# Kernel optimization log

Measured on AMD Instinct MI355X. Metric: run time of the kernel, lower is better.

The kernel has to match this reference:

```python
import jax, jax.numpy as jnp
import numpy as np

DIM = 2048
N_HEADS = 16
HEAD_DIM = DIM // N_HEADS
ROPE_BASE = 10000.0


def _rope_cos_sin(seq_len, head_dim, dtype):
    inv_freq = 1.0 / (ROPE_BASE ** (jnp.arange(0, head_dim, 2, dtype=jnp.float32) / head_dim))
    t = jnp.arange(seq_len, dtype=jnp.float32)
    freqs = jnp.einsum('s,d->sd', t, inv_freq)          # (S, hd/2)
    emb = jnp.concatenate([freqs, freqs], axis=-1)       # (S, hd)
    return jnp.cos(emb).astype(dtype), jnp.sin(emb).astype(dtype)


def _rotate_half(x):
    x1, x2 = jnp.split(x, 2, axis=-1)
    return jnp.concatenate([-x2, x1], axis=-1)


def _apply_rope(x, cos, sin):
    # x: (B, H, S, hd); cos/sin: (S, hd)
    return x * cos[None, None] + _rotate_half(x) * sin[None, None]


def setup_inputs() -> dict:
    key = jax.random.key(0)
    ks = jax.random.split(key, 5)
    B, S = 2, 2048
    scale = 1.0 / np.sqrt(DIM)
    return {
        'x': jax.random.normal(ks[0], (B, S, DIM), dtype=jnp.float32),
        'Wq': jax.random.normal(ks[1], (DIM, DIM), dtype=jnp.float32) * scale,
        'Wk': jax.random.normal(ks[2], (DIM, DIM), dtype=jnp.float32) * scale,
        'Wv': jax.random.normal(ks[3], (DIM, DIM), dtype=jnp.float32) * scale,
        'Wo': jax.random.normal(ks[4], (DIM, DIM), dtype=jnp.float32) * scale,
    }


def reference(x, Wq, Wk, Wv, Wo):
    B, S, _ = x.shape
    scale = HEAD_DIM ** -0.5

    def proj(W):
        # torch Linear: x @ W.T ; reshape to (B, H, S, hd)
        return (x @ W.T).reshape(B, S, N_HEADS, HEAD_DIM).transpose(0, 2, 1, 3)

    q, k, v = proj(Wq), proj(Wk), proj(Wv)
    cos, sin = _rope_cos_sin(S, HEAD_DIM, x.dtype)
    q = _apply_rope(q, cos, sin)
    k = _apply_rope(k, cos, sin)

    scores = jnp.einsum('bhqd,bhkd->bhqk', q, k) * scale  # (B,H,S,S)
    causal = jnp.triu(jnp.ones((S, S), dtype=bool), k=1)
    scores = jnp.where(causal[None, None], -jnp.inf, scores)
    attn = jax.nn.softmax(scores.astype(jnp.float32), axis=-1).astype(q.dtype)
    out = jnp.einsum('bhqk,bhkd->bhqd', attn, v)          # (B,H,S,hd)
    out = out.transpose(0, 2, 1, 3).reshape(B, S, DIM)
    return out @ Wo.T
```

## Files before the change

kernel.cpp:

```cpp
#include <hip/hip_runtime.h>


#define SEQ 2048
#define DMODEL 2048
#define NH 16
#define HD 128

typedef __attribute__((ext_vector_type(8))) short bf16x8;
typedef __attribute__((ext_vector_type(4))) float f32x4;

__device__ __forceinline__ unsigned short f2bf(float f) {
  unsigned int u = __float_as_uint(f);
  u += 0x7fffu + ((u >> 16) & 1u);
  return (unsigned short)(u >> 16);
}

__device__ __forceinline__ void g2l16(const void* g, void* l) {
  __builtin_amdgcn_global_load_lds((const __attribute__((address_space(1))) void*)g,
                                   (__attribute__((address_space(3))) void*)l,
                                   16, 0, 0);
}

__device__ __forceinline__ f32x4 mfma16(bf16x8 a, bf16x8 b, f32x4 c) {
  return __builtin_amdgcn_mfma_f32_16x16x32_bf16(a, b, c, 0, 0, 0);
}

template <int CTRL>
__device__ __forceinline__ float dpp_ror(float v) {
  return __int_as_float(__builtin_amdgcn_mov_dpp(__float_as_int(v), CTRL, 0xf, 0xf, false));
}
__device__ __forceinline__ float red_max16(float v) {
  v = fmaxf(v, dpp_ror<0x128>(v));
  v = fmaxf(v, dpp_ror<0x124>(v));
  v = fmaxf(v, dpp_ror<0x122>(v));
  v = fmaxf(v, dpp_ror<0x121>(v));
  return v;
}
__device__ __forceinline__ float red_sum16(float v) {
  v += dpp_ror<0x128>(v);
  v += dpp_ror<0x124>(v);
  v += dpp_ror<0x122>(v);
  v += dpp_ror<0x121>(v);
  return v;
}

__global__ __launch_bounds__(256) void cvt_all(const float* __restrict__ x,
                                               const float* __restrict__ wq,
                                               const float* __restrict__ wk,
                                               const float* __restrict__ wv,
                                               const float* __restrict__ wo,
                                               unsigned short* __restrict__ dst0) {
  const int b = blockIdx.x;
  const float* src;
  unsigned short* dst;
  int idx;
  if (b < 8192) {
    src = x; dst = dst0; idx = b * 256 + threadIdx.x;
  } else {
    const int r = (b - 8192) >> 12;
    src = (r == 0) ? wq : (r == 1) ? wk : (r == 2) ? wv : wo;
    dst = dst0 + (size_t)2 * SEQ * DMODEL + (size_t)r * DMODEL * DMODEL;
    idx = ((b - 8192) & 4095) * 256 + threadIdx.x;
  }
  const float4 v = ((const float4*)src)[idx];
  ushort4 o;
  o.x = f2bf(v.x); o.y = f2bf(v.y); o.z = f2bf(v.z); o.w = f2bf(v.w);
  ((ushort4*)dst)[idx] = o;
}


__global__ __launch_bounds__(256) void gemm_qkv(
    const unsigned short* __restrict__ X,
    const unsigned short* __restrict__ Wq,
    const unsigned short* __restrict__ Wk,
    const unsigned short* __restrict__ Wv,
    unsigned short* __restrict__ Qo,
    unsigned short* __restrict__ Ko,
    unsigned short* __restrict__ Vo) {
  __shared__ unsigned short As[128 * 64];
  __shared__ unsigned short Bs[128 * 64];
  const int z = blockIdx.z;
  const unsigned short* W = (z == 0) ? Wq : (z == 1) ? Wk : Wv;
  const int M0 = blockIdx.y * 128;
  const int h = blockIdx.x;
  const int N0 = h * 128;
  const int t = threadIdx.x;
  const int w = t >> 6, lane = t & 63, l15 = lane & 15, quad = lane >> 4;
  const int g = lane >> 3, j = lane & 7;
  const int chunk = j ^ g;

  f32x4 acc[2][8] = {};

  for (int k0 = 0; k0 < DMODEL; k0 += 64) {
    __syncthreads();
#pragma unroll
    for (int r = 0; r < 8; ++r) {
      const int u = r * 4 + w;
      const int row = (u & 15) * 8 + g;
      if (u < 16)
        g2l16(X + (size_t)(M0 + row) * DMODEL + k0 + chunk * 8, &As[(u & 15) * 512]);
      else
        g2l16(W + (size_t)(N0 + row) * DMODEL + k0 + chunk * 8, &Bs[(u & 15) * 512]);
    }
    __syncthreads();
#pragma unroll
    for (int kc = 0; kc < 2; ++kc) {
      const int c = kc * 4 + quad;
      bf16x8 af[2];
#pragma unroll
      for (int mt = 0; mt < 2; ++mt) {
        const int m = w * 32 + mt * 16 + l15;
        af[mt] = *(const bf16x8*)&As[m * 64 + ((c ^ (m & 7)) << 3)];
      }
#pragma unroll
      for (int nt = 0; nt < 8; ++nt) {
        const int n = nt * 16 + l15;
        const bf16x8 bv = *(const bf16x8*)&Bs[n * 64 + ((c ^ (n & 7)) << 3)];
#pragma unroll
        for (int mt = 0; mt < 2; ++mt) acc[mt][nt] = mfma16(af[mt], bv, acc[mt][nt]);
      }
    }
  }

  if (z < 2) {
    const float qscale = (z == 0) ? 0.1275174356f : 1.0f;
    float invf[4];
#pragma unroll
    for (int jj = 0; jj < 4; ++jj)
      invf[jj] = exp2f(-0.20762050593046f * (float)(jj * 16 + l15));
    unsigned short* O = (z == 0) ? Qo : Ko;
#pragma unroll
    for (int mt = 0; mt < 2; ++mt)
#pragma unroll
      for (int reg = 0; reg < 4; ++reg) {
        const int m = M0 + w * 32 + mt * 16 + quad * 4 + reg;
        const int b = m >> 11, s = m & 2047;
        unsigned short* ob = O + ((size_t)(b * NH + h) * SEQ + s) * HD;
        const float fs = (float)s;
#pragma unroll
        for (int jj = 0; jj < 4; ++jj) {
          float sn, cs;
          sincosf(fs * invf[jj], &sn, &cs);
          const float x1 = acc[mt][jj][reg], x2 = acc[mt][jj + 4][reg];
          ob[jj * 16 + l15] = f2bf((x1 * cs - x2 * sn) * qscale);
          ob[64 + jj * 16 + l15] = f2bf((x2 * cs + x1 * sn) * qscale);
        }
      }
  } else {
#pragma unroll
    for (int mt = 0; mt < 2; ++mt)
#pragma unroll
      for (int reg = 0; reg < 4; ++reg) {
        const int m = M0 + w * 32 + mt * 16 + quad * 4 + reg;
        const int b = m >> 11, s = m & 2047;
        unsigned short* ob = Vo + (size_t)(b * NH + h) * HD * SEQ;
#pragma unroll
        for (int nt = 0; nt < 8; ++nt)
          ob[(size_t)(nt * 16 + l15) * SEQ + s] = f2bf(acc[mt][nt][reg]);
      }
  }
}

__global__ __launch_bounds__(256) void attn_kernel(const unsigned short* __restrict__ Q,
                                                   const unsigned short* __restrict__ K,
                                                   const unsigned short* __restrict__ Vt,
                                                   unsigned short* __restrict__ Oa) {
  __shared__ unsigned short Ks[256 * 64];
  __shared__ unsigned short Vs[256 * 64];
  const int gid = blockIdx.x;
  const int bh = gid & 31;
  const int pr = gid >> 5;
  const unsigned short* Qb = Q + (size_t)bh * SEQ * HD;
  const unsigned short* Kb = K + (size_t)bh * SEQ * HD;
  const unsigned short* Vb = Vt + (size_t)bh * HD * SEQ;
  const int t = threadIdx.x;
  const int w = t >> 6, lane = t & 63, l15 = lane & 15, quad = lane >> 4;
  const int g = lane >> 3, j = lane & 7;
  const int b = bh >> 4, h = bh & 15;

  for (int half = 0; half < 2; ++half) {
    const int qt = half ? 15 - pr : pr;

    bf16x8 qf[2][4];
#pragma unroll
    for (int mt = 0; mt < 2; ++mt)
#pragma unroll
      for (int ch = 0; ch < 4; ++ch)
        qf[mt][ch] = *(const bf16x8*)(Qb + (size_t)(qt * 128 + w * 32 + mt * 16 + l15) * HD +
                                      ch * 32 + quad * 8);

    f32x4 o[2][8] = {};
    float mrow[2][4], lrow[2][4];
#pragma unroll
    for (int mt = 0; mt < 2; ++mt)
#pragma unroll
      for (int reg = 0; reg < 4; ++reg) { mrow[mt][reg] = -1e30f; lrow[mt][reg] = 0.f; }

    for (int kt = 0; kt <= qt; ++kt) {
      __syncthreads();
#pragma unroll
      for (int r = 0; r < 16; ++r) {
        const int u = r * 4 + w;
        if (u < 32) {
          const int vrow = u * 8 + g, key = vrow >> 1;
          const int ck = j ^ (key & 7);
          g2l16(Kb + (size_t)(kt * 128 + key) * HD + (vrow & 1) * 64 + ck * 8, &Ks[u * 512]);
        } else {
          const int u2 = u - 32;
          const int vrow = u2 * 8 + g, d = vrow >> 1;
          const int cv = j ^ (d & 7);
          g2l16(Vb + (size_t)d * SEQ + kt * 128 + (vrow & 1) * 64 + cv * 8, &Vs[u2 * 512]);
        }
      }
      __syncthreads();

      f32x4 s[2][8] = {};
#pragma unroll
      for (int ch = 0; ch < 4; ++ch) {
        const int hh = ch >> 1, c = (ch & 1) * 4 + quad;
#pragma unroll
        for (int nt = 0; nt < 8; ++nt) {
          const int n = nt * 16 + l15;
          const bf16x8 bv = *(const bf16x8*)&Ks[(n * 2 + hh) * 64 + ((c ^ (n & 7)) << 3)];
#pragma unroll
          for (int mt = 0; mt < 2; ++mt) s[mt][nt] = mfma16(qf[mt][ch], bv, s[mt][nt]);
        }
      }

      if (kt == qt) {
#pragma unroll
        for (int mt = 0; mt < 2; ++mt)
#pragma unroll
          for (int nt = 0; nt < 8; ++nt)
#pragma unroll
            for (int reg = 0; reg < 4; ++reg) {
              const int rr = w * 32 + mt * 16 + quad * 4 + reg;
              const int cc = nt * 16 + l15;
              if (cc > rr) s[mt][nt][reg] = -1e30f;
            }
      }

#pragma unroll
      for (int mt = 0; mt < 2; ++mt)
#pragma unroll
        for (int reg = 0; reg < 4; ++reg) {
          float vmax = s[mt][0][reg];
#pragma unroll
          for (int nt = 1; nt < 8; ++nt) vmax = fmaxf(vmax, s[mt][nt][reg]);
          vmax = red_max16(vmax);
          const float mo = mrow[mt][reg];
          const float mn = fmaxf(mo, vmax);
          const float alpha = exp2f(mo - mn);
          mrow[mt][reg] = mn;
          float rs = 0.f;
#pragma unroll
          for (int nt = 0; nt < 8; ++nt) {
            const float p_ = exp2f(s[mt][nt][reg] - mn);
            s[mt][nt][reg] = p_;
            rs += p_;
          }
          rs = red_sum16(rs);
          lrow[mt][reg] = lrow[mt][reg] * alpha + rs;
#pragma unroll
          for (int nt = 0; nt < 8; ++nt) o[mt][nt][reg] *= alpha;
        }

      __syncthreads();

      unsigned short* Pw = &Ks[w * 4096];
#pragma unroll
      for (int mt = 0; mt < 2; ++mt)
#pragma unroll
        for (int nt = 0; nt < 8; ++nt)
#pragma unroll
          for (int reg = 0; reg < 4; ++reg) {
            const int rr = mt * 16 + quad * 4 + reg;
            const int key = nt * 16 + l15;
            Pw[(key >> 3) * 256 + rr * 8 + (key & 7)] = f2bf(s[mt][nt][reg]);
          }

#pragma unroll
      for (int ch = 0; ch < 4; ++ch) {
        const int kh = ch >> 1, c = (ch & 1) * 4 + quad;
        bf16x8 pa[2];
#pragma unroll
        for (int mt = 0; mt < 2; ++mt)
          pa[mt] = *(const bf16x8*)&Pw[(ch * 4 + quad) * 256 + (mt * 16 + l15) * 8];
#pragma unroll
        for (int nt = 0; nt < 8; ++nt) {
          const int d = nt * 16 + l15;
          const bf16x8 vv = *(const bf16x8*)&Vs[(d * 2 + kh) * 64 + ((c ^ (d & 7)) << 3)];
#pragma unroll
          for (int mt = 0; mt < 2; ++mt) o[mt][nt] = mfma16(pa[mt], vv, o[mt][nt]);
        }
      }
    }

#pragma unroll
    for (int mt = 0; mt < 2; ++mt)
#pragma unroll
      for (int reg = 0; reg < 4; ++reg) {
        const int sq = qt * 128 + w * 32 + mt * 16 + quad * 4 + reg;
        const float inv_l = 1.0f / lrow[mt][reg];
        unsigned short* ob = Oa + (size_t)(b * SEQ + sq) * DMODEL + h * HD;
#pragma unroll
        for (int nt = 0; nt < 8; ++nt) ob[nt * 16 + l15] = f2bf(o[mt][nt][reg] * inv_l);
      }
  }
}

__global__ __launch_bounds__(256) void gemm_out(const unsigned short* __restrict__ A,
                                                const unsigned short* __restrict__ W,
                                                float* __restrict__ out) {
  __shared__ unsigned short As[128 * 64];
  __shared__ unsigned short Bs[128 * 64];
  const int M0 = blockIdx.y * 128;
  const int N0 = blockIdx.x * 128;
  const int t = threadIdx.x;
  const int w = t >> 6, lane = t & 63, l15 = lane & 15, quad = lane >> 4;
  const int g = lane >> 3, j = lane & 7;
  const int chunk = j ^ g;

  f32x4 acc[2][8] = {};

  for (int k0 = 0; k0 < DMODEL; k0 += 64) {
    __syncthreads();
#pragma unroll
    for (int r = 0; r < 8; ++r) {
      const int u = r * 4 + w;
      const int row = (u & 15) * 8 + g;
      if (u < 16)
        g2l16(A + (size_t)(M0 + row) * DMODEL + k0 + chunk * 8, &As[(u & 15) * 512]);
      else
        g2l16(W + (size_t)(N0 + row) * DMODEL + k0 + chunk * 8, &Bs[(u & 15) * 512]);
    }
    __syncthreads();
#pragma unroll
    for (int kc = 0; kc < 2; ++kc) {
      const int c = kc * 4 + quad;
      bf16x8 af[2];
#pragma unroll
      for (int mt = 0; mt < 2; ++mt) {
        const int m = w * 32 + mt * 16 + l15;
        af[mt] = *(const bf16x8*)&As[m * 64 + ((c ^ (m & 7)) << 3)];
      }
#pragma unroll
      for (int nt = 0; nt < 8; ++nt) {
        const int n = nt * 16 + l15;
        const bf16x8 bv = *(const bf16x8*)&Bs[n * 64 + ((c ^ (n & 7)) << 3)];
#pragma unroll
        for (int mt = 0; mt < 2; ++mt) acc[mt][nt] = mfma16(af[mt], bv, acc[mt][nt]);
      }
    }
  }

#pragma unroll
  for (int mt = 0; mt < 2; ++mt)
#pragma unroll
    for (int nt = 0; nt < 8; ++nt)
#pragma unroll
      for (int reg = 0; reg < 4; ++reg) {
        const int m = M0 + w * 32 + mt * 16 + quad * 4 + reg;
        out[(size_t)m * DMODEL + N0 + nt * 16 + l15] = acc[mt][nt][reg];
      }
}

extern "C" void kernel_launch(void* const* d_in, const int* in_sizes, int n_in,
                              void* d_out, int out_size, void* d_ws, size_t ws_size,
                              hipStream_t stream) {
  const float* x = (const float*)d_in[0];
  const float* Wq = (const float*)d_in[1];
  const float* Wk = (const float*)d_in[2];
  const float* Wv = (const float*)d_in[3];
  const float* Wo = (const float*)d_in[4];
  float* out = (float*)d_out;

  const size_t NX = (size_t)2 * SEQ * DMODEL;
  const size_t NW = (size_t)DMODEL * DMODEL;
  unsigned short* ws = (unsigned short*)d_ws;
  unsigned short* xb = ws;
  unsigned short* wqb = xb + NX;
  unsigned short* wkb = wqb + NW;
  unsigned short* wvb = wkb + NW;
  unsigned short* wob = wvb + NW;
  unsigned short* qb = wob + NW;
  unsigned short* kb = qb + NX;
  unsigned short* vb = kb + NX;
  unsigned short* ab = vb + NX;

  cvt_all<<<24576, 256, 0, stream>>>(x, Wq, Wk, Wv, Wo, ws);
  gemm_qkv<<<dim3(16, 32, 3), 256, 0, stream>>>(xb, wqb, wkb, wvb, qb, kb, vb);
  attn_kernel<<<256, 256, 0, stream>>>(qb, kb, vb, ab);
  gemm_out<<<dim3(16, 32, 1), 256, 0, stream>>>(ab, wob, out);
}
```

Measured before the change: 413.4 us.

## Replace QKV and output GEMMs with triple-buffered 256x128 pipelined GEMM and RoPE table

Both projection GEMMs now use one templated kernel with 512 threads, 256x128 tiles and a three-stage LDS ring. Global-to-LDS loads for tile k+2 are issued while tile k is computed, and waitcnt/barrier are placed by hand, replacing the load-then-sync loop. The Wq/Wk rows are permuted during bf16 conversion so each wave holds matching rotate-half pairs for RoPE. Cos/sin come from a table precomputed in the conversion kernel rather than per-element sincosf. QKV now runs as a single 48x16 grid using contiguous Q/K/V workspace, which adds LDS pressure and relies on exact vmcnt counting.

```diff
diff --git a/kernel.cpp b/kernel.cpp
--- a/kernel.cpp
+++ b/kernel.cpp
@@ -49,15 +49,24 @@
                                                const float* __restrict__ wk,
                                                const float* __restrict__ wv,
                                                const float* __restrict__ wo,
-                                               unsigned short* __restrict__ dst0) {
+                                               unsigned short* __restrict__ dst0,
+                                               float2* __restrict__ rtab) {
   const int b = blockIdx.x;
+  if (b >= 24576) {
+    const int idx = (b - 24576) * 256 + threadIdx.x;
+    const int s = idx >> 6, d = idx & 63;
+    float sn, cs;
+    sincosf((float)s * exp2f(-0.20762050593046f * (float)d), &sn, &cs);
+    rtab[idx] = make_float2(cs, sn);
+    return;
+  }
   const float* src;
   unsigned short* dst;
-  int idx;
+  int idx, r = -1;
   if (b < 8192) {
     src = x; dst = dst0; idx = b * 256 + threadIdx.x;
   } else {
-    const int r = (b - 8192) >> 12;
+    r = (b - 8192) >> 12;
     src = (r == 0) ? wq : (r == 1) ? wk : (r == 2) ? wv : wo;
     dst = dst0 + (size_t)2 * SEQ * DMODEL + (size_t)r * DMODEL * DMODEL;
     idx = ((b - 8192) & 4095) * 256 + threadIdx.x;
@@ -65,98 +74,143 @@
   const float4 v = ((const float4*)src)[idx];
   ushort4 o;
   o.x = f2bf(v.x); o.y = f2bf(v.y); o.z = f2bf(v.z); o.w = f2bf(v.w);
-  ((ushort4*)dst)[idx] = o;
-}
-
-
-__global__ __launch_bounds__(256) void gemm_qkv(
-    const unsigned short* __restrict__ X,
-    const unsigned short* __restrict__ Wq,
-    const unsigned short* __restrict__ Wk,
-    const unsigned short* __restrict__ Wv,
-    unsigned short* __restrict__ Qo,
-    unsigned short* __restrict__ Ko,
-    unsigned short* __restrict__ Vo) {
-  __shared__ unsigned short As[128 * 64];
-  __shared__ unsigned short Bs[128 * 64];
-  const int z = blockIdx.z;
-  const unsigned short* W = (z == 0) ? Wq : (z == 1) ? Wk : Wv;
-  const int M0 = blockIdx.y * 128;
-  const int h = blockIdx.x;
-  const int N0 = h * 128;
+  int widx = idx;
+  if (r == 0 || r == 1) {
+    const int row = idx >> 9, col = idx & 511;
+    const int o_ = row & 127;
+    const int e = (((o_ >> 4) & 3) << 5) | (((o_ >> 6) & 1) << 4) | (o_ & 15);
+    widx = (((row & ~127) | e) << 9) | col;
+  }
+  ((ushort4*)dst)[widx] = o;
+}
+
+template <int MODE>
+__global__ __launch_bounds__(512, 2) void gemm_pipe(
+    const unsigned short* __restrict__ A,
+    const unsigned short* __restrict__ B,
+    unsigned short* __restrict__ obf,
+    float* __restrict__ of32,
+    const float2* __restrict__ rtab) {
+  __shared__ unsigned short lds[3 * 24576];
+  const int nb = blockIdx.x, mb = blockIdx.y;
+  const int M0 = mb * 256;
   const int t = threadIdx.x;
   const int w = t >> 6, lane = t & 63, l15 = lane & 15, quad = lane >> 4;
   const int g = lane >> 3, j = lane & 7;
-  const int chunk = j ^ g;
-
-  f32x4 acc[2][8] = {};
-
-  for (int k0 = 0; k0 < DMODEL; k0 += 64) {
-    __syncthreads();
-#pragma unroll
-    for (int r = 0; r < 8; ++r) {
-      const int u = r * 4 + w;
-      const int row = (u & 15) * 8 + g;
-      if (u < 16)
-        g2l16(X + (size_t)(M0 + row) * DMODEL + k0 + chunk * 8, &As[(u & 15) * 512]);
-      else
-        g2l16(W + (size_t)(N0 + row) * DMODEL + k0 + chunk * 8, &Bs[(u & 15) * 512]);
-    }
-    __syncthreads();
-#pragma unroll
-    for (int kc = 0; kc < 2; ++kc) {
-      const int c = kc * 4 + quad;
-      bf16x8 af[2];
-#pragma unroll
-      for (int mt = 0; mt < 2; ++mt) {
-        const int m = w * 32 + mt * 16 + l15;
-        af[mt] = *(const bf16x8*)&As[m * 64 + ((c ^ (m & 7)) << 3)];
-      }
-#pragma unroll
-      for (int nt = 0; nt < 8; ++nt) {
-        const int n = nt * 16 + l15;
-        const bf16x8 bv = *(const bf16x8*)&Bs[n * 64 + ((c ^ (n & 7)) << 3)];
-#pragma unroll
-        for (int mt = 0; mt < 2; ++mt) acc[mt][nt] = mfma16(af[mt], bv, acc[mt][nt]);
-      }
-    }
-  }
-
-  if (z < 2) {
-    const float qscale = (z == 0) ? 0.1275174356f : 1.0f;
-    float invf[4];
-#pragma unroll
-    for (int jj = 0; jj < 4; ++jj)
-      invf[jj] = exp2f(-0.20762050593046f * (float)(jj * 16 + l15));
-    unsigned short* O = (z == 0) ? Qo : Ko;
-#pragma unroll
-    for (int mt = 0; mt < 2; ++mt)
+  const int wm = w >> 1, wn = w & 1;
+
+  const unsigned short* Abase = A + (size_t)M0 * DMODEL;
+  const unsigned short* Bbase = B + (size_t)nb * 128 * DMODEL;
+
+  f32x4 acc[4][4] = {};
+
+  auto stage = [&](int buf, int k0, int i0) {
+#pragma unroll
+    for (int i = 0; i < 3; ++i) {
+      const int u = w * 6 + i0 + i;
+      if (u < 32) {
+        const int row = u * 8 + g;
+        g2l16(Abase + (size_t)row * DMODEL + k0 + ((j ^ g) << 3),
+              &lds[buf * 24576 + u * 512]);
+      } else {
+        const int row = (u - 32) * 8 + g;
+        g2l16(Bbase + (size_t)row * DMODEL + k0 + ((j ^ g) << 3),
+              &lds[buf * 24576 + 16384 + (u - 32) * 512]);
+      }
+    }
+  };
+
+  auto comp = [&](int buf, int kc) {
+    const int c = kc * 4 + quad;
+    const unsigned short* As_ = &lds[buf * 24576];
+    const unsigned short* Bs_ = &lds[buf * 24576 + 16384];
+    bf16x8 af[4], bf[4];
+#pragma unroll
+    for (int mt = 0; mt < 4; ++mt) {
+      const int m = wm * 64 + mt * 16 + l15;
+      af[mt] = *(const bf16x8*)&As_[m * 64 + ((c ^ (m & 7)) << 3)];
+    }
+#pragma unroll
+    for (int nt = 0; nt < 4; ++nt) {
+      const int n = wn * 64 + nt * 16 + l15;
+      bf[nt] = *(const bf16x8*)&Bs_[n * 64 + ((c ^ (n & 7)) << 3)];
+    }
+#pragma unroll
+    for (int nt = 0; nt < 4; ++nt)
+#pragma unroll
+      for (int mt = 0; mt < 4; ++mt)
+        acc[mt][nt] = mfma16(af[mt], bf[nt], acc[mt][nt]);
+  };
+
+  stage(0, 0, 0);
+  stage(0, 0, 3);
+  stage(1, 64, 0);
+  stage(1, 64, 3);
+  asm volatile("s_waitcnt vmcnt(6)\n\ts_barrier" ::: "memory");
+
+  int buf = 0, b2 = 2;
+  for (int tt = 0; tt < 32; ++tt) {
+    const int k0 = tt * 64;
+    if (tt < 30) stage(b2, k0 + 128, 0);
+    comp(buf, 0);
+    if (tt < 30) stage(b2, k0 + 128, 3);
+    comp(buf, 1);
+    if (tt < 30) {
+      asm volatile("s_waitcnt vmcnt(6)\n\ts_barrier" ::: "memory");
+    } else if (tt == 30) {
+      asm volatile("s_waitcnt vmcnt(0)\n\ts_barrier" ::: "memory");
+    }
+    buf = (buf == 2) ? 0 : buf + 1;
+    b2 = (b2 == 2) ? 0 : b2 + 1;
+  }
+
+  if (MODE == 0) {
+    const size_t NX = (size_t)2 * SEQ * DMODEL;
+    const int z = nb >> 4;
+    const int h = nb & 15;
+    if (z < 2) {
+      const float qscale = (z == 0) ? 0.1275174356f : 1.0f;
+      unsigned short* O = obf + (size_t)z * NX;
+#pragma unroll
+      for (int mt = 0; mt < 4; ++mt)
+#pragma unroll
+        for (int reg = 0; reg < 4; ++reg) {
+          const int m = M0 + wm * 64 + mt * 16 + quad * 4 + reg;
+          const int bb = m >> 11, s = m & 2047;
+          unsigned short* ob = O + ((size_t)(bb * NH + h) * SEQ + s) * HD;
+#pragma unroll
+          for (int p = 0; p < 2; ++p) {
+            const int q = wn * 2 + p;
+            const float2 cs = rtab[s * 64 + q * 16 + l15];
+            const float x1 = acc[mt][2 * p][reg], x2 = acc[mt][2 * p + 1][reg];
+            ob[wn * 64 + (2 * p) * 16 + l15] = f2bf((x1 * cs.x - x2 * cs.y) * qscale);
+            ob[wn * 64 + (2 * p + 1) * 16 + l15] = f2bf((x2 * cs.x + x1 * cs.y) * qscale);
+          }
+        }
+    } else {
+      unsigned short* Vb = obf + 2 * NX + (size_t)h * HD * SEQ;
+#pragma unroll
+      for (int mt = 0; mt < 4; ++mt)
+#pragma unroll
+        for (int reg = 0; reg < 4; ++reg) {
+          const int m = M0 + wm * 64 + mt * 16 + quad * 4 + reg;
+          const int bb = m >> 11, s = m & 2047;
+          unsigned short* ob = Vb + (size_t)bb * NH * HD * SEQ;
+#pragma unroll
+          for (int nt = 0; nt < 4; ++nt)
+            ob[(size_t)(wn * 64 + nt * 16 + l15) * SEQ + s] = f2bf(acc[mt][nt][reg]);
+        }
+    }
+  } else {
+#pragma unroll
+    for (int mt = 0; mt < 4; ++mt)
 #pragma unroll
       for (int reg = 0; reg < 4; ++reg) {
-        const int m = M0 + w * 32 + mt * 16 + quad * 4 + reg;
-        const int b = m >> 11, s = m & 2047;
-        unsigned short* ob = O + ((size_t)(b * NH + h) * SEQ + s) * HD;
-        const float fs = (float)s;
-#pragma unroll
-        for (int jj = 0; jj < 4; ++jj) {
-          float sn, cs;
-          sincosf(fs * invf[jj], &sn, &cs);
-          const float x1 = acc[mt][jj][reg], x2 = acc[mt][jj + 4][reg];
-          ob[jj * 16 + l15] = f2bf((x1 * cs - x2 * sn) * qscale);
-          ob[64 + jj * 16 + l15] = f2bf((x2 * cs + x1 * sn) * qscale);
-        }
-      }
-  } else {
-#pragma unroll
-    for (int mt = 0; mt < 2; ++mt)
-#pragma unroll
-      for (int reg = 0; reg < 4; ++reg) {
-        const int m = M0 + w * 32 + mt * 16 + quad * 4 + reg;
-        const int b = m >> 11, s = m & 2047;
-        unsigned short* ob = Vo + (size_t)(b * NH + h) * HD * SEQ;
-#pragma unroll
-        for (int nt = 0; nt < 8; ++nt)
-          ob[(size_t)(nt * 16 + l15) * SEQ + s] = f2bf(acc[mt][nt][reg]);
+        const int m = M0 + wm * 64 + mt * 16 + quad * 4 + reg;
+#pragma unroll
+        for (int nt = 0; nt < 4; ++nt)
+          of32[(size_t)m * DMODEL + nb * 128 + wn * 64 + nt * 16 + l15] =
+              acc[mt][nt][reg];
       }
   }
 }
@@ -309,62 +363,6 @@
   }
 }
 
-__global__ __launch_bounds__(256) void gemm_out(const unsigned short* __restrict__ A,
-                                                const unsigned short* __restrict__ W,
-                                                float* __restrict__ out) {
-  __shared__ unsigned short As[128 * 64];
-  __shared__ unsigned short Bs[128 * 64];
-  const int M0 = blockIdx.y * 128;
-  const int N0 = blockIdx.x * 128;
-  const int t = threadIdx.x;
-  const int w = t >> 6, lane = t & 63, l15 = lane & 15, quad = lane >> 4;
-  const int g = lane >> 3, j = lane & 7;
-  const int chunk = j ^ g;
-
-  f32x4 acc[2][8] = {};
-
-  for (int k0 = 0; k0 < DMODEL; k0 += 64) {
-    __syncthreads();
-#pragma unroll
-    for (int r = 0; r < 8; ++r) {
-      const int u = r * 4 + w;
-      const int row = (u & 15) * 8 + g;
-      if (u < 16)
-        g2l16(A + (size_t)(M0 + row) * DMODEL + k0 + chunk * 8, &As[(u & 15) * 512]);
-      else
-        g2l16(W + (size_t)(N0 + row) * DMODEL + k0 + chunk * 8, &Bs[(u & 15) * 512]);
-    }
-    __syncthreads();
-#pragma unroll
-    for (int kc = 0; kc < 2; ++kc) {
-      const int c = kc * 4 + quad;
-      bf16x8 af[2];
-#pragma unroll
-      for (int mt = 0; mt < 2; ++mt) {
-        const int m = w * 32 + mt * 16 + l15;
-        af[mt] = *(const bf16x8*)&As[m * 64 + ((c ^ (m & 7)) << 3)];
-      }
-#pragma unroll
-      for (int nt = 0; nt < 8; ++nt) {
-        const int n = nt * 16 + l15;
-        const bf16x8 bv = *(const bf16x8*)&Bs[n * 64 + ((c ^ (n & 7)) << 3)];
-#pragma unroll
-        for (int mt = 0; mt < 2; ++mt) acc[mt][nt] = mfma16(af[mt], bv, acc[mt][nt]);
-      }
-    }
-  }
-
-#pragma unroll
-  for (int mt = 0; mt < 2; ++mt)
-#pragma unroll
-    for (int nt = 0; nt < 8; ++nt)
-#pragma unroll
-      for (int reg = 0; reg < 4; ++reg) {
-        const int m = M0 + w * 32 + mt * 16 + quad * 4 + reg;
-        out[(size_t)m * DMODEL + N0 + nt * 16 + l15] = acc[mt][nt][reg];
-      }
-}
-
 extern "C" void kernel_launch(void* const* d_in, const int* in_sizes, int n_in,
                               void* d_out, int out_size, void* d_ws, size_t ws_size,
                               hipStream_t stream) {
@@ -387,9 +385,10 @@
   unsigned short* kb = qb + NX;
   unsigned short* vb = kb + NX;
   unsigned short* ab = vb + NX;
-
-  cvt_all<<<24576, 256, 0, stream>>>(x, Wq, Wk, Wv, Wo, ws);
-  gemm_qkv<<<dim3(16, 32, 3), 256, 0, stream>>>(xb, wqb, wkb, wvb, qb, kb, vb);
+  float2* rtab = (float2*)(ab + NX);
+
+  cvt_all<<<25088, 256, 0, stream>>>(x, Wq, Wk, Wv, Wo, ws, rtab);
+  gemm_pipe<0><<<dim3(48, 16), 512, 0, stream>>>(xb, wqb, qb, nullptr, rtab);
   attn_kernel<<<256, 256, 0, stream>>>(qb, kb, vb, ab);
-  gemm_out<<<dim3(16, 32, 1), 256, 0, stream>>>(ab, wob, out);
-}
+  gemm_pipe<1><<<dim3(16, 16), 512, 0, stream>>>(ab, wob, nullptr, out, nullptr);
+}
```

Result: faster. 371.5 us (-10.1%).
